# Kernel optimization log

Hardware: AMD Instinct MI355X
Metric: run time of the kernel (lower is better)

Reference implementation:

```python
import jax, jax.numpy as jnp
import numpy as np
from jax import lax

EPS = 1e-6
CLAMP = 1e4


def _ln_last(x, w, b):
    # fp32 LayerNorm over last dim
    mu = jnp.mean(x, axis=-1, keepdims=True)
    var = jnp.mean(jnp.square(x - mu), axis=-1, keepdims=True)
    return (x - mu) * lax.rsqrt(var + EPS) * w + b


def _nan_clean(x):
    return jnp.nan_to_num(x, nan=0.0, posinf=CLAMP, neginf=-CLAMP)


def setup_inputs() -> dict:
    key = jax.random.key(0)
    B, C, H, W = 4, 256, 64, 64
    hid = 2 * C  # expand=2
    k = 3        # d_conv
    ks = jax.random.split(key, 12)
    s = 0.02
    return {
        "x": jax.random.normal(ks[0], (B, C, H, W), jnp.float32),
        "ln2d_w": jnp.ones((C,), jnp.float32),
        "ln2d_b": jnp.zeros((C,), jnp.float32),
        "inproj_w": jax.random.normal(ks[1], (C, C), jnp.float32) * s,
        "inproj_b": jnp.zeros((C,), jnp.float32),
        "dw2d_w": jax.random.normal(ks[2], (C, 3, 3), jnp.float32) * s,
        "dw2d_b": jnp.zeros((C,), jnp.float32),
        "ssm_ln_w": jnp.ones((C,), jnp.float32),
        "ssm_ln_b": jnp.zeros((C,), jnp.float32),
        "ssm_in_w": jax.random.normal(ks[3], (2 * hid, C), jnp.float32) * s,
        "ssm_in_b": jnp.zeros((2 * hid,), jnp.float32),
        "ssm_dw_w": jax.random.normal(ks[4], (hid, k), jnp.float32) * s,
        "ssm_dw_b": jnp.zeros((hid,), jnp.float32),
        "ssm_out_w": jax.random.normal(ks[5], (C, hid), jnp.float32) * s,
        "ssm_out_b": jnp.zeros((C,), jnp.float32),
        "outproj_w": jax.random.normal(ks[6], (C, C), jnp.float32) * s,
        "outproj_b": jnp.zeros((C,), jnp.float32),
    }


def reference(x, ln2d_w, ln2d_b, inproj_w, inproj_b, dw2d_w, dw2d_b,
              ssm_ln_w, ssm_ln_b, ssm_in_w, ssm_in_b, ssm_dw_w, ssm_dw_b,
              ssm_out_w, ssm_out_b, outproj_w, outproj_b):
    B, C, H, W = x.shape
    L = H * W

    # LN2d over channel dim (per-pixel LN on C)
    y = _ln_last(x.transpose(0, 2, 3, 1), ln2d_w, ln2d_b).transpose(0, 3, 1, 2)

    # 1x1 conv in_proj
    y = jnp.einsum('bchw,oc->bohw', y, inproj_w) + inproj_b[None, :, None, None]

    # depthwise 3x3 conv, SAME padding
    y = lax.conv_general_dilated(
        y, dw2d_w[:, None, :, :], (1, 1), ((1, 1), (1, 1)),
        dimension_numbers=('NCHW', 'OIHW', 'NCHW'),
        feature_group_count=C) + dw2d_b[None, :, None, None]

    # cross-scan: 4 routes (B,L,C)
    s0 = y.reshape(B, C, L).transpose(0, 2, 1)                      # row-major
    s1 = s0[:, ::-1]                                                # reversed
    s2 = y.transpose(0, 1, 3, 2).reshape(B, C, L).transpose(0, 2, 1)  # col-major
    s3 = s2[:, ::-1]
    s = jnp.concatenate([s0, s1, s2, s3], axis=0)  # (4B, L, C), shared SSM weights

    # MambaOrLite fallback: LN -> GLU -> depthwise conv1d -> out proj + residual
    r = _ln_last(s, ssm_ln_w, ssm_ln_b)
    r = r @ ssm_in_w.T + ssm_in_b                   # (4B, L, 2*hid)
    a, g = jnp.split(r, 2, axis=-1)
    r = a * jax.nn.sigmoid(g)                       # (4B, L, hid)
    r = r.transpose(0, 2, 1)                        # (4B, hid, L)
    hid = r.shape[1]
    k = ssm_dw_w.shape[-1]
    pad = ((k - 1) // 2, k // 2)
    r = lax.conv_general_dilated(
        r, ssm_dw_w[:, None, :], (1,), (pad,),
        dimension_numbers=('NCH', 'OIH', 'NCH'),
        feature_group_count=hid) + ssm_dw_b[None, :, None]
    r = r.transpose(0, 2, 1) @ ssm_out_w.T + ssm_out_b  # (4B, L, C)
    ys = _nan_clean(r) + s

    # cross-merge: average the 4 routes back to (B,C,H,W)
    y0, y1, y2, y3 = jnp.split(ys, 4, axis=0)
    m0 = y0.transpose(0, 2, 1).reshape(B, C, H, W)
    m1 = y1[:, ::-1].transpose(0, 2, 1).reshape(B, C, H, W)
    m2 = y2.transpose(0, 2, 1).reshape(B, C, W, H).transpose(0, 1, 3, 2)
    m3 = y3[:, ::-1].transpose(0, 2, 1).reshape(B, C, W, H).transpose(0, 1, 3, 2)
    m = (m0 + m1 + m2 + m3) * 0.25

    out = jnp.einsum('bchw,oc->bohw', m, outproj_w) + outproj_b[None, :, None, None]
    out = _nan_clean(out)
    return out + x
```

## Files before the change

### kernel.cpp

```cpp
#include <hip/hip_runtime.h>

typedef float f32x4 __attribute__((ext_vector_type(4)));
typedef __bf16 bf16x8 __attribute__((ext_vector_type(8)));
typedef unsigned short u16;
typedef unsigned int u32;

__device__ __forceinline__ float bf2f(u32 b) {
  u32 x = (b & 0xffffu) << 16;
  return __builtin_bit_cast(float, x);
}
__device__ __forceinline__ u16 f2bf(float f) {
  u32 x = __builtin_bit_cast(u32, f);
  x += 0x7fffu + ((x >> 16) & 1u);
  return (u16)(x >> 16);
}
__device__ __forceinline__ void gload16(const void* g, void* l) {
  __builtin_amdgcn_global_load_lds((__attribute__((address_space(1))) void*)g,
                                   (__attribute__((address_space(3))) void*)l,
                                   16, 0, 0);
}
__device__ __forceinline__ int xcd_swz(int bid, int nwg) {
  int per = nwg >> 3;
  return (bid & 7) * per + (bid >> 3);
}

__global__ __launch_bounds__(256, 2)
void k_ln2d_prep(const float* __restrict__ x, const float* __restrict__ lw,
                 const float* __restrict__ lb, u16* __restrict__ A,
                 const float* __restrict__ inproj_w, const float* __restrict__ ssm_in_w,
                 const float* __restrict__ ssm_out_w, const float* __restrict__ outproj_w,
                 const float* __restrict__ dw2d_w, const float* __restrict__ ssm_dw_w,
                 const float* __restrict__ ssm_dw_b, const float* __restrict__ ssm_out_b,
                 u16* __restrict__ w1b, u16* __restrict__ w2b, u16* __restrict__ w3b,
                 u16* __restrict__ w4b, float* __restrict__ cvec, float* __restrict__ wT9,
                 float* __restrict__ w02, float* __restrict__ w14) {
  __shared__ float T[256 * 65];
  __shared__ float ps1[4][64], ps2[4][64];
  __shared__ float mu[64], rsd[64];
  int bid = blockIdx.x, tid = threadIdx.x;
  if (bid >= 256) {
    int pb = bid - 256;
    if (pb < 512) {
      const float* s; u16* d; int base;
      if (pb < 256)      { s = ssm_in_w;  d = w2b; base = pb; }
      else if (pb < 384) { s = ssm_out_w; d = w3b; base = pb - 256; }
      else if (pb < 448) { s = inproj_w;  d = w1b; base = pb - 384; }
      else               { s = outproj_w; d = w4b; base = pb - 448; }
      int i = base * 1024 + tid * 4;
      float4 v = *(const float4*)&s[i];
      u32 a = (u32)f2bf(v.x) | ((u32)f2bf(v.y) << 16);
      u32 b = (u32)f2bf(v.z) | ((u32)f2bf(v.w) << 16);
      *(uint2*)&d[i] = make_uint2(a, b);
    } else if (pb == 512) {
      float s = ssm_out_b[tid];
      const float* wr = ssm_out_w + (size_t)tid * 512;
      #pragma unroll 8
      for (int k = 0; k < 512; ++k) s += ssm_dw_b[k] * wr[k];
      cvec[tid] = s;
    } else {
      #pragma unroll
      for (int j = 0; j < 9; ++j) wT9[j * 256 + tid] = dw2d_w[tid * 9 + j];
      #pragma unroll
      for (int q = 0; q < 2; ++q) {
        int c = tid + q * 256;
        w02[c] = ssm_dw_w[c * 3 + 0] + ssm_dw_w[c * 3 + 2];
        w14[c] = 4.f * ssm_dw_w[c * 3 + 1];
      }
    }
    return;
  }
  int wv = tid >> 6, lane = tid & 63;
  int cq = lane >> 4, p4 = (lane & 15) * 4;
  int n0 = bid * 64, bb = n0 >> 12, hw0 = n0 & 4095;
  const float* xb = x + ((size_t)bb << 20);
  float s0 = 0, s1 = 0, s2 = 0, s3 = 0;
  float q0 = 0, q1 = 0, q2 = 0, q3 = 0;
  #pragma unroll 4
  for (int i = 0; i < 16; ++i) {
    int c = wv * 64 + i * 4 + cq;
    float4 v = *(const float4*)&xb[((size_t)c << 12) + hw0 + p4];
    T[c * 65 + p4 + 0] = v.x; T[c * 65 + p4 + 1] = v.y;
    T[c * 65 + p4 + 2] = v.z; T[c * 65 + p4 + 3] = v.w;
    s0 += v.x; s1 += v.y; s2 += v.z; s3 += v.w;
    q0 += v.x * v.x; q1 += v.y * v.y; q2 += v.z * v.z; q3 += v.w * v.w;
  }
  #pragma unroll
  for (int off = 16; off < 64; off <<= 1) {
    s0 += __shfl_xor(s0, off); s1 += __shfl_xor(s1, off);
    s2 += __shfl_xor(s2, off); s3 += __shfl_xor(s3, off);
    q0 += __shfl_xor(q0, off); q1 += __shfl_xor(q1, off);
    q2 += __shfl_xor(q2, off); q3 += __shfl_xor(q3, off);
  }
  if (cq == 0) {
    ps1[wv][p4 + 0] = s0; ps1[wv][p4 + 1] = s1; ps1[wv][p4 + 2] = s2; ps1[wv][p4 + 3] = s3;
    ps2[wv][p4 + 0] = q0; ps2[wv][p4 + 1] = q1; ps2[wv][p4 + 2] = q2; ps2[wv][p4 + 3] = q3;
  }
  __syncthreads();
  if (tid < 64) {
    float S1 = ps1[0][tid] + ps1[1][tid] + ps1[2][tid] + ps1[3][tid];
    float S2 = ps2[0][tid] + ps2[1][tid] + ps2[2][tid] + ps2[3][tid];
    float m = S1 * (1.f / 256.f);
    float var = S2 * (1.f / 256.f) - m * m;
    mu[tid] = m;
    rsd[tid] = rsqrtf(var + 1e-6f);
  }
  __syncthreads();
  int c4b = (tid & 15) * 4, p2b = tid >> 4;
  #pragma unroll
  for (int cc = 0; cc < 4; ++cc) {
    int c4 = cc * 64 + c4b;
    float4 w4 = *(const float4*)&lw[c4];
    float4 g4 = *(const float4*)&lb[c4];
    #pragma unroll
    for (int i2 = 0; i2 < 4; ++i2) {
      int p2 = p2b + 16 * i2;
      float m = mu[p2], rs = rsd[p2];
      float o0 = (T[(c4 + 0) * 65 + p2] - m) * rs * w4.x + g4.x;
      float o1 = (T[(c4 + 1) * 65 + p2] - m) * rs * w4.y + g4.y;
      float o2 = (T[(c4 + 2) * 65 + p2] - m) * rs * w4.z + g4.z;
      float o3 = (T[(c4 + 3) * 65 + p2] - m) * rs * w4.w + g4.w;
      u32 a = (u32)f2bf(o0) | ((u32)f2bf(o1) << 16);
      u32 b = (u32)f2bf(o2) | ((u32)f2bf(o3) << 16);
      *(uint2*)&A[(size_t)(n0 + p2) * 256 + c4] = make_uint2(a, b);
    }
  }
}

__global__ __launch_bounds__(256, 4)
void k_gemm_in(const u16* __restrict__ R, const u16* __restrict__ Cm,
               const float* __restrict__ bias, u16* __restrict__ outb) {
  __shared__ u16 tR[2][64 * 32];
  __shared__ u16 tC[2][128 * 32];
  int tid = threadIdx.x, lane = tid & 63, wv = tid >> 6;
  const int K = 256;
  int rt = blockIdx.x >> 1, ct = blockIdx.x & 1;
  int r0 = rt * 64, c0 = ct * 128;
  int fr = lane & 15, kc = lane >> 4;
  int sr = lane >> 2, sc = (lane & 3) * 8;
  f32x4 acc[4][2] = {};
  const u16* gR  = R  + (size_t)(r0 + wv * 16 + sr) * K + sc;
  const u16* gC0 = Cm + (size_t)(c0 + wv * 32 + sr) * K + sc;
  const u16* gC1 = Cm + (size_t)(c0 + wv * 32 + 16 + sr) * K + sc;
  auto STAGE = [&](int buf, int kt) {
    int k0 = kt * 32;
    gload16(gR + k0,  &tR[buf][wv * 16 * 32]);
    gload16(gC0 + k0, &tC[buf][(wv * 32) * 32]);
    gload16(gC1 + k0, &tC[buf][(wv * 32 + 16) * 32]);
  };
  auto COMPUTE = [&](int buf) {
    bf16x8 af[4], wf[2];
    #pragma unroll
    for (int m = 0; m < 4; ++m)
      af[m] = *(const bf16x8*)&tR[buf][(m * 16 + fr) * 32 + kc * 8];
    #pragma unroll
    for (int n = 0; n < 2; ++n)
      wf[n] = *(const bf16x8*)&tC[buf][(wv * 32 + n * 16 + fr) * 32 + kc * 8];
    #pragma unroll
    for (int m = 0; m < 4; ++m)
      #pragma unroll
      for (int n = 0; n < 2; ++n)
        acc[m][n] = __builtin_amdgcn_mfma_f32_16x16x32_bf16(af[m], wf[n], acc[m][n], 0, 0, 0);
  };
  STAGE(0, 0);
  __syncthreads();
  int cur = 0;
  for (int kt = 0; kt < 7; ++kt) {
    STAGE(cur ^ 1, kt + 1);
    __builtin_amdgcn_sched_barrier(0);
    COMPUTE(cur);
    __syncthreads();
    cur ^= 1;
  }
  COMPUTE(cur);
  #pragma unroll
  for (int m = 0; m < 4; ++m) {
    #pragma unroll
    for (int n = 0; n < 2; ++n) {
      #pragma unroll
      for (int r = 0; r < 4; ++r) {
        int gn = r0 + m * 16 + kc * 4 + r;
        int go = c0 + wv * 32 + n * 16 + fr;
        outb[(size_t)gn * 256 + go] = f2bf(acc[m][n][r] + bias[go]);
      }
    }
  }
}

__global__ __launch_bounds__(256)
void k_dw3x3_ln(const u16* __restrict__ Y1, const float* __restrict__ wT,
                const float* __restrict__ dwb, const float* __restrict__ lnw,
                const float* __restrict__ lnb, u16* __restrict__ Yc,
                u16* __restrict__ A) {
  int tid = threadIdx.x;
  int wg = xcd_swz(blockIdx.x, 4096);
  int n = wg * 4 + (tid >> 6);
  int lane = tid & 63;
  int c0 = lane * 4;
  int b = n >> 12, hw = n & 4095, h = hw >> 6, w = hw & 63;
  float4 b4 = *(const float4*)&dwb[c0];
  float a0 = b4.x, a1 = b4.y, a2 = b4.z, a3 = b4.w;
  #pragma unroll
  for (int ky = 0; ky < 3; ++ky) {
    int hh = h + ky - 1;
    if (hh < 0 || hh > 63) continue;
    #pragma unroll
    for (int kx = 0; kx < 3; ++kx) {
      int ww = w + kx - 1;
      if (ww < 0 || ww > 63) continue;
      size_t nn = ((size_t)b << 12) + (hh << 6) + ww;
      uint2 u = *(const uint2*)&Y1[nn * 256 + c0];
      float4 w4 = *(const float4*)&wT[(ky * 3 + kx) * 256 + c0];
      a0 += bf2f(u.x) * w4.x;
      a1 += bf2f(u.x >> 16) * w4.y;
      a2 += bf2f(u.y) * w4.z;
      a3 += bf2f(u.y >> 16) * w4.w;
    }
  }
  u32 p0 = (u32)f2bf(a0) | ((u32)f2bf(a1) << 16);
  u32 p1 = (u32)f2bf(a2) | ((u32)f2bf(a3) << 16);
  *(uint2*)&Yc[(size_t)n * 256 + c0] = make_uint2(p0, p1);
  float s1 = a0 + a1 + a2 + a3;
  float s2 = a0 * a0 + a1 * a1 + a2 * a2 + a3 * a3;
  #pragma unroll
  for (int off = 1; off < 64; off <<= 1) {
    s1 += __shfl_xor(s1, off);
    s2 += __shfl_xor(s2, off);
  }
  float m = s1 * (1.f / 256.f);
  float var = s2 * (1.f / 256.f) - m * m;
  float rs = rsqrtf(var + 1e-6f);
  float4 w4 = *(const float4*)&lnw[c0];
  float4 g4 = *(const float4*)&lnb[c0];
  float o0 = (a0 - m) * rs * w4.x + g4.x;
  float o1 = (a1 - m) * rs * w4.y + g4.y;
  float o2 = (a2 - m) * rs * w4.z + g4.z;
  float o3 = (a3 - m) * rs * w4.w + g4.w;
  u32 qa = (u32)f2bf(o0) | ((u32)f2bf(o1) << 16);
  u32 qb = (u32)f2bf(o2) | ((u32)f2bf(o3) << 16);
  *(uint2*)&A[(size_t)n * 256 + c0] = make_uint2(qa, qb);
}

__global__ __launch_bounds__(256, 3)
void k_gate2(const u16* __restrict__ A, const u16* __restrict__ W,
             const float* __restrict__ bias, u16* __restrict__ G) {
  __shared__ u16 tR[2][64 * 32];
  __shared__ u16 tCa[2][128 * 32];
  __shared__ u16 tCg[2][128 * 32];
  int tid = threadIdx.x, lane = tid & 63, wv = tid >> 6;
  int rt = blockIdx.x >> 2, ot = blockIdx.x & 3;
  int r0 = rt * 64, o0 = ot * 128;
  int fr = lane & 15, kc = lane >> 4;
  int sr = lane >> 2, sc = (lane & 3) * 8;
  const int K = 256;
  f32x4 acca[4][2] = {}, accg[4][2] = {};
  const u16* gR  = A + (size_t)(r0 + wv * 16 + sr) * K + sc;
  const u16* gA0 = W + (size_t)(o0 + wv * 32 + sr) * K + sc;
  const u16* gA1 = W + (size_t)(o0 + wv * 32 + 16 + sr) * K + sc;
  const u16* gG0 = W + (size_t)(512 + o0 + wv * 32 + sr) * K + sc;
  const u16* gG1 = W + (size_t)(512 + o0 + wv * 32 + 16 + sr) * K + sc;
  auto STAGE = [&](int buf, int kt) {
    int k0 = kt * 32;
    gload16(gR + k0,  &tR[buf][wv * 16 * 32]);
    gload16(gA0 + k0, &tCa[buf][(wv * 32) * 32]);
    gload16(gA1 + k0, &tCa[buf][(wv * 32 + 16) * 32]);
    gload16(gG0 + k0, &tCg[buf][(wv * 32) * 32]);
    gload16(gG1 + k0, &tCg[buf][(wv * 32 + 16) * 32]);
  };
  auto COMPUTE = [&](int buf) {
    bf16x8 af[4], wa[2], wg[2];
    #pragma unroll
    for (int m = 0; m < 4; ++m)
      af[m] = *(const bf16x8*)&tR[buf][(m * 16 + fr) * 32 + kc * 8];
    #pragma unroll
    for (int n = 0; n < 2; ++n) {
      wa[n] = *(const bf16x8*)&tCa[buf][(wv * 32 + n * 16 + fr) * 32 + kc * 8];
      wg[n] = *(const bf16x8*)&tCg[buf][(wv * 32 + n * 16 + fr) * 32 + kc * 8];
    }
    #pragma unroll
    for (int m = 0; m < 4; ++m)
      #pragma unroll
      for (int n = 0; n < 2; ++n) {
        acca[m][n] = __builtin_amdgcn_mfma_f32_16x16x32_bf16(af[m], wa[n], acca[m][n], 0, 0, 0);
        accg[m][n] = __builtin_amdgcn_mfma_f32_16x16x32_bf16(af[m], wg[n], accg[m][n], 0, 0, 0);
      }
  };
  STAGE(0, 0);
  __syncthreads();
  int cur = 0;
  for (int kt = 0; kt < 7; ++kt) {
    STAGE(cur ^ 1, kt + 1);
    __builtin_amdgcn_sched_barrier(0);
    COMPUTE(cur);
    __syncthreads();
    cur ^= 1;
  }
  COMPUTE(cur);
  #pragma unroll
  for (int m = 0; m < 4; ++m) {
    #pragma unroll
    for (int n = 0; n < 2; ++n) {
      #pragma unroll
      for (int r = 0; r < 4; ++r) {
        int gn = r0 + m * 16 + kc * 4 + r;
        int go = o0 + wv * 32 + n * 16 + fr;
        float a = acca[m][n][r] + bias[go];
        float g = accg[m][n][r] + bias[512 + go];
        G[(size_t)gn * 512 + go] = f2bf(a / (1.f + expf(-g)));
      }
    }
  }
}

__global__ __launch_bounds__(256, 2)
void k_scan_out(const u16* __restrict__ G, const u16* __restrict__ W3,
                const float* __restrict__ w02, const float* __restrict__ w14,
                const float* __restrict__ cvec, const u16* __restrict__ Yc,
                const u16* __restrict__ W4, const float* __restrict__ outb,
                const float* __restrict__ xres, float* __restrict__ out) {
  __shared__ u16 tR[2][32 * 32];
  __shared__ u16 tC[2][256 * 32];
  __shared__ u16 sM[32 * 256];
  int tid = threadIdx.x, lane = tid & 63, wv = tid >> 6;
  int wg = xcd_swz(blockIdx.x, 512);
  int r0 = wg * 32;
  int fr = lane & 15, kc = lane >> 4;
  int zrow = tid >> 3;
  int zg = (tid & 7) * 4;
  int n = r0 + zrow;
  int b = n >> 12, hw = n & 4095, h = hw >> 6, w = hw & 63;
  int m = w * 64 + h;
  int mm1 = m - 1, mp1 = m + 1;
  size_t o_c = (size_t)n * 512 + zg;
  size_t o_p = (size_t)(hw > 0 ? n - 1 : n) * 512 + zg;
  size_t o_n = (size_t)(hw < 4095 ? n + 1 : n) * 512 + zg;
  size_t o_u = (size_t)(m > 0 ? ((b << 12) + ((mm1 & 63) << 6) + (mm1 >> 6)) : n) * 512 + zg;
  size_t o_d = (size_t)(m < 4095 ? ((b << 12) + ((mp1 & 63) << 6) + (mp1 >> 6)) : n) * 512 + zg;
  float mP = hw > 0 ? 1.f : 0.f, mN = hw < 4095 ? 1.f : 0.f;
  float mU = m > 0 ? 1.f : 0.f, mD = m < 4095 ? 1.f : 0.f;
  f32x4 acc[2][4] = {};
  auto STAGE_C = [&](int buf, int kt) {
    int k0 = kt * 32;
    #pragma unroll
    for (int i = 0; i < 4; ++i) {
      int s0 = wv * 256 + i * 64;
      int s = s0 + lane;
      int row = s >> 2, off = (s & 3) * 8;
      gload16(W3 + (size_t)row * 512 + k0 + off, &tC[buf][s0 * 8]);
    }
  };
  uint2 lc, lp, ln_, lu, ld;
  float4 va, vb;
  auto ZLOAD = [&](int kt) {
    int c = kt * 32 + zg;
    lc  = *(const uint2*)&G[o_c + (kt * 32)];
    lp  = *(const uint2*)&G[o_p + (kt * 32)];
    ln_ = *(const uint2*)&G[o_n + (kt * 32)];
    lu  = *(const uint2*)&G[o_u + (kt * 32)];
    ld  = *(const uint2*)&G[o_d + (kt * 32)];
    va = *(const float4*)&w02[c];
    vb = *(const float4*)&w14[c];
  };
  auto ZSTORE = [&](int buf) {
    float s_0 = mP * bf2f(lp.x) + mN * bf2f(ln_.x) + mU * bf2f(lu.x) + mD * bf2f(ld.x);
    float s_1 = mP * bf2f(lp.x >> 16) + mN * bf2f(ln_.x >> 16) + mU * bf2f(lu.x >> 16) + mD * bf2f(ld.x >> 16);
    float s_2 = mP * bf2f(lp.y) + mN * bf2f(ln_.y) + mU * bf2f(lu.y) + mD * bf2f(ld.y);
    float s_3 = mP * bf2f(lp.y >> 16) + mN * bf2f(ln_.y >> 16) + mU * bf2f(lu.y >> 16) + mD * bf2f(ld.y >> 16);
    float z0 = va.x * s_0 + vb.x * bf2f(lc.x);
    float z1 = va.y * s_1 + vb.y * bf2f(lc.x >> 16);
    float z2 = va.z * s_2 + vb.z * bf2f(lc.y);
    float z3 = va.w * s_3 + vb.w * bf2f(lc.y >> 16);
    u32 p0 = (u32)f2bf(z0) | ((u32)f2bf(z1) << 16);
    u32 p1 = (u32)f2bf(z2) | ((u32)f2bf(z3) << 16);
    *(uint2*)&tR[buf][zrow * 32 + zg] = make_uint2(p0, p1);
  };
  auto COMPUTE = [&](int buf) {
    bf16x8 af[2], wf[4];
    #pragma unroll
    for (int mi = 0; mi < 2; ++mi)
      af[mi] = *(const bf16x8*)&tR[buf][(mi * 16 + fr) * 32 + kc * 8];
    #pragma unroll
    for (int ni = 0; ni < 4; ++ni)
      wf[ni] = *(const bf16x8*)&tC[buf][(wv * 64 + ni * 16 + fr) * 32 + kc * 8];
    #pragma unroll
    for (int mi = 0; mi < 2; ++mi)
      #pragma unroll
      for (int ni = 0; ni < 4; ++ni)
        acc[mi][ni] = __builtin_amdgcn_mfma_f32_16x16x32_bf16(af[mi], wf[ni], acc[mi][ni], 0, 0, 0);
  };
  STAGE_C(0, 0);
  ZLOAD(0);
  ZSTORE(0);
  __syncthreads();
  int cur = 0;
  for (int kt = 0; kt < 15; ++kt) {
    ZLOAD(kt + 1);
    STAGE_C(cur ^ 1, kt + 1);
    COMPUTE(cur);
    ZSTORE(cur ^ 1);
    __syncthreads();
    cur ^= 1;
  }
  COMPUTE(cur);
  #pragma unroll
  for (int mi = 0; mi < 2; ++mi) {
    #pragma unroll
    for (int ni = 0; ni < 4; ++ni) {
      #pragma unroll
      for (int r = 0; r < 4; ++r) {
        int row = mi * 16 + kc * 4 + r;
        int go = wv * 64 + ni * 16 + fr;
        float mval = 0.25f * acc[mi][ni][r] + cvec[go] +
                     bf2f(Yc[(size_t)(r0 + row) * 256 + go]);
        u32 ba = ((u32)(row * 512 + go * 2)) ^ ((u32)(row & 7) << 4);
        *(u16*)((char*)sM + ba) = f2bf(mval);
      }
    }
  }
  __syncthreads();
  f32x4 acc2[4][2] = {};
  #pragma unroll 2
  for (int kt = 0; kt < 8; ++kt) {
    bf16x8 af2[4], bfv[2];
    #pragma unroll
    for (int mi = 0; mi < 4; ++mi)
      af2[mi] = *(const bf16x8*)&W4[(size_t)(wv * 64 + mi * 16 + fr) * 256 + kt * 32 + kc * 8];
    #pragma unroll
    for (int ni = 0; ni < 2; ++ni) {
      int pos = ni * 16 + fr;
      u32 ba = ((u32)(pos * 512 + (kt * 32 + kc * 8) * 2)) ^ ((u32)(pos & 7) << 4);
      bfv[ni] = *(const bf16x8*)((const char*)sM + ba);
    }
    #pragma unroll
    for (int mi = 0; mi < 4; ++mi)
      #pragma unroll
      for (int ni = 0; ni < 2; ++ni)
        acc2[mi][ni] = __builtin_amdgcn_mfma_f32_16x16x32_bf16(af2[mi], bfv[ni], acc2[mi][ni], 0, 0, 0);
  }
  int bb = r0 >> 12, hwb = r0 & 4095;
  #pragma unroll
  for (int mi = 0; mi < 4; ++mi) {
    #pragma unroll
    for (int ni = 0; ni < 2; ++ni) {
      #pragma unroll
      for (int r = 0; r < 4; ++r) {
        int o = wv * 64 + mi * 16 + kc * 4 + r;
        int pos = ni * 16 + fr;
        size_t idx = (((size_t)(bb * 256 + o)) << 12) + hwb + pos;
        float res = __builtin_nontemporal_load(&xres[idx]);
        __builtin_nontemporal_store(acc2[mi][ni][r] + outb[o] + res, &out[idx]);
      }
    }
  }
}

extern "C" void kernel_launch(void* const* d_in, const int* in_sizes, int n_in,
                              void* d_out, int out_size, void* d_ws, size_t ws_size,
                              hipStream_t stream) {
  const float* x         = (const float*)d_in[0];
  const float* ln2d_w    = (const float*)d_in[1];
  const float* ln2d_b    = (const float*)d_in[2];
  const float* inproj_w  = (const float*)d_in[3];
  const float* inproj_b  = (const float*)d_in[4];
  const float* dw2d_w    = (const float*)d_in[5];
  const float* dw2d_b    = (const float*)d_in[6];
  const float* ssm_ln_w  = (const float*)d_in[7];
  const float* ssm_ln_b  = (const float*)d_in[8];
  const float* ssm_in_w  = (const float*)d_in[9];
  const float* ssm_in_b  = (const float*)d_in[10];
  const float* ssm_dw_w  = (const float*)d_in[11];
  const float* ssm_dw_b  = (const float*)d_in[12];
  const float* ssm_out_w = (const float*)d_in[13];
  const float* ssm_out_b = (const float*)d_in[14];
  const float* outproj_w = (const float*)d_in[15];
  const float* outproj_b = (const float*)d_in[16];
  float* out = (float*)d_out;

  char* ws = (char*)d_ws;
  size_t off = 0;
  auto take = [&](size_t bytes) -> char* {
    char* p = ws + off;
    off = (off + bytes + 255) & ~(size_t)255;
    return p;
  };
  u16* w1b    = (u16*)take(65536 * 2);
  u16* w2b    = (u16*)take(262144 * 2);
  u16* w3b    = (u16*)take(131072 * 2);
  u16* w4b    = (u16*)take(65536 * 2);
  float* cvec = (float*)take(256 * 4);
  float* wT9  = (float*)take(9 * 256 * 4);
  float* w02  = (float*)take(512 * 4);
  float* w14  = (float*)take(512 * 4);
  u16* Abuf   = (u16*)take((size_t)16384 * 256 * 2);
  u16* Y1     = (u16*)take((size_t)16384 * 256 * 2);
  u16* Yc     = (u16*)take((size_t)16384 * 256 * 2);
  u16* G      = (u16*)take((size_t)16384 * 512 * 2);
  (void)ws_size; (void)in_sizes; (void)n_in; (void)out_size;

  k_ln2d_prep<<<770, 256, 0, stream>>>(x, ln2d_w, ln2d_b, Abuf,
                                       inproj_w, ssm_in_w, ssm_out_w, outproj_w,
                                       dw2d_w, ssm_dw_w, ssm_dw_b, ssm_out_b,
                                       w1b, w2b, w3b, w4b, cvec, wT9, w02, w14);
  k_gemm_in<<<512, 256, 0, stream>>>(Abuf, w1b, inproj_b, Y1);
  k_dw3x3_ln<<<4096, 256, 0, stream>>>(Y1, wT9, dw2d_b, ssm_ln_w, ssm_ln_b, Yc, Abuf);
  k_gate2<<<1024, 256, 0, stream>>>(Abuf, w2b, ssm_in_b, G);
  k_scan_out<<<512, 256, 0, stream>>>(G, w3b, w02, w14, cvec, Yc,
                                      w4b, outproj_b, x, out);
}
```

Baseline: 109.6 us.

## Replace in-proj and gate GEMMs with row-tile kernel looping over all output columns

Both the in_proj GEMM and the gated ssm_in GEMM are replaced by one templated kernel. Each block now loads a 32-row slab of activations into LDS once and loops over all output column tiles, streaming weight tiles through a double buffer, so activation rows are read from global memory only once. LDS uses XOR-swizzled layouts to avoid bank conflicts, and outputs are staged in LDS for coalesced 16-byte stores. The price is smaller per-block MFMA tiles (2x2), more LDS per block and lower occupancy, plus repeated weight re-reads per block.

```diff
diff --git a/kernel.cpp b/kernel.cpp
--- a/kernel.cpp
+++ b/kernel.cpp
@@ -126,63 +126,102 @@
   }
 }
 
-__global__ __launch_bounds__(256, 4)
-void k_gemm_in(const u16* __restrict__ R, const u16* __restrict__ Cm,
-               const float* __restrict__ bias, u16* __restrict__ outb) {
-  __shared__ u16 tR[2][64 * 32];
-  __shared__ u16 tC[2][128 * 32];
+template <int NOT, bool GATE>
+__global__ __launch_bounds__(256, 2)
+void k_colgemm(const u16* __restrict__ A, const u16* __restrict__ W,
+               const float* __restrict__ bias, u16* __restrict__ Out) {
+  constexpr int COLS = NOT * 128;
+  __shared__ u16 sA[32 * 256];
+  __shared__ u16 tCa[2][128 * 32];
+  __shared__ u16 tCg[(GATE ? 2 : 1)][128 * 32];
+  __shared__ u16 sO[32 * COLS];
   int tid = threadIdx.x, lane = tid & 63, wv = tid >> 6;
-  const int K = 256;
-  int rt = blockIdx.x >> 1, ct = blockIdx.x & 1;
-  int r0 = rt * 64, c0 = ct * 128;
+  int r0 = blockIdx.x * 32;
   int fr = lane & 15, kc = lane >> 4;
-  int sr = lane >> 2, sc = (lane & 3) * 8;
-  f32x4 acc[4][2] = {};
-  const u16* gR  = R  + (size_t)(r0 + wv * 16 + sr) * K + sc;
-  const u16* gC0 = Cm + (size_t)(c0 + wv * 32 + sr) * K + sc;
-  const u16* gC1 = Cm + (size_t)(c0 + wv * 32 + 16 + sr) * K + sc;
-  auto STAGE = [&](int buf, int kt) {
-    int k0 = kt * 32;
-    gload16(gR + k0,  &tR[buf][wv * 16 * 32]);
-    gload16(gC0 + k0, &tC[buf][(wv * 32) * 32]);
-    gload16(gC1 + k0, &tC[buf][(wv * 32 + 16) * 32]);
-  };
-  auto COMPUTE = [&](int buf) {
-    bf16x8 af[4], wf[2];
-    #pragma unroll
-    for (int m = 0; m < 4; ++m)
-      af[m] = *(const bf16x8*)&tR[buf][(m * 16 + fr) * 32 + kc * 8];
-    #pragma unroll
-    for (int n = 0; n < 2; ++n)
-      wf[n] = *(const bf16x8*)&tC[buf][(wv * 32 + n * 16 + fr) * 32 + kc * 8];
-    #pragma unroll
-    for (int m = 0; m < 4; ++m)
-      #pragma unroll
-      for (int n = 0; n < 2; ++n)
-        acc[m][n] = __builtin_amdgcn_mfma_f32_16x16x32_bf16(af[m], wf[n], acc[m][n], 0, 0, 0);
-  };
-  STAGE(0, 0);
-  __syncthreads();
-  int cur = 0;
-  for (int kt = 0; kt < 7; ++kt) {
-    STAGE(cur ^ 1, kt + 1);
-    __builtin_amdgcn_sched_barrier(0);
-    COMPUTE(cur);
-    __syncthreads();
-    cur ^= 1;
-  }
-  COMPUTE(cur);
-  #pragma unroll
-  for (int m = 0; m < 4; ++m) {
-    #pragma unroll
-    for (int n = 0; n < 2; ++n) {
-      #pragma unroll
-      for (int r = 0; r < 4; ++r) {
-        int gn = r0 + m * 16 + kc * 4 + r;
-        int go = c0 + wv * 32 + n * 16 + fr;
-        outb[(size_t)gn * 256 + go] = f2bf(acc[m][n][r] + bias[go]);
-      }
-    }
+  #pragma unroll
+  for (int j = 0; j < 4; ++j) {
+    int Gi0 = j * 256 + wv * 64;
+    int Gi = Gi0 + lane;
+    int row = Gi >> 5, g = Gi & 31;
+    gload16(A + (size_t)(r0 + row) * 256 + ((g ^ (row & 7)) << 3), &sA[Gi0 * 8]);
+  }
+  auto STAGE_W = [&](int buf, int ot, int kt) {
+    #pragma unroll
+    for (int j = 0; j < 2; ++j) {
+      int Gi0 = j * 256 + wv * 64;
+      int Gi = Gi0 + lane;
+      int row = Gi >> 2, g = Gi & 3;
+      int gs = (g ^ ((row >> 1) & 3)) << 3;
+      gload16(W + (size_t)(ot * 128 + row) * 256 + kt * 32 + gs, &tCa[buf][Gi0 * 8]);
+      if constexpr (GATE)
+        gload16(W + (size_t)(512 + ot * 128 + row) * 256 + kt * 32 + gs, &tCg[buf][Gi0 * 8]);
+    }
+  };
+  STAGE_W(0, 0, 0);
+  __syncthreads();
+  int buf = 0;
+  for (int ot = 0; ot < NOT; ++ot) {
+    f32x4 aA[2][2] = {};
+    f32x4 aG[2][2] = {};
+    for (int kt = 0; kt < 8; ++kt) {
+      int np = ot * 8 + kt + 1;
+      if (np < NOT * 8) STAGE_W(buf ^ 1, np >> 3, np & 7);
+      __builtin_amdgcn_sched_barrier(0);
+      bf16x8 af[2], wa[2], wg[2];
+      #pragma unroll
+      for (int m = 0; m < 2; ++m) {
+        int row = m * 16 + fr;
+        af[m] = *(const bf16x8*)&sA[row * 256 + (((kt * 4 + kc) ^ (fr & 7)) << 3)];
+      }
+      int wgs = (kc ^ ((fr >> 1) & 3)) << 3;
+      #pragma unroll
+      for (int n = 0; n < 2; ++n) {
+        int row = wv * 32 + n * 16 + fr;
+        wa[n] = *(const bf16x8*)&tCa[buf][row * 32 + wgs];
+        if constexpr (GATE)
+          wg[n] = *(const bf16x8*)&tCg[buf][row * 32 + wgs];
+      }
+      #pragma unroll
+      for (int m = 0; m < 2; ++m)
+        #pragma unroll
+        for (int n = 0; n < 2; ++n) {
+          aA[m][n] = __builtin_amdgcn_mfma_f32_16x16x32_bf16(af[m], wa[n], aA[m][n], 0, 0, 0);
+          if constexpr (GATE)
+            aG[m][n] = __builtin_amdgcn_mfma_f32_16x16x32_bf16(af[m], wg[n], aG[m][n], 0, 0, 0);
+        }
+      __syncthreads();
+      buf ^= 1;
+    }
+    #pragma unroll
+    for (int m = 0; m < 2; ++m) {
+      #pragma unroll
+      for (int n = 0; n < 2; ++n) {
+        #pragma unroll
+        for (int r = 0; r < 4; ++r) {
+          int row = m * 16 + kc * 4 + r;
+          int go = ot * 128 + wv * 32 + n * 16 + fr;
+          float v;
+          if constexpr (GATE) {
+            float a = aA[m][n][r] + bias[go];
+            float g = aG[m][n][r] + bias[512 + go];
+            v = a / (1.f + expf(-g));
+          } else {
+            v = aA[m][n][r] + bias[go];
+          }
+          sO[row * COLS + go] = f2bf(v);
+        }
+      }
+    }
+  }
+  __syncthreads();
+  constexpr int GPR = COLS / 8;
+  constexpr int NG = 32 * GPR;
+  #pragma unroll
+  for (int j = 0; j < NG / 256; ++j) {
+    int Gi = j * 256 + wv * 64 + lane;
+    int row = Gi / GPR, cg = Gi % GPR;
+    uint4 v = *(const uint4*)&sO[Gi * 8];
+    *(uint4*)&Out[(size_t)(r0 + row) * COLS + cg * 8] = v;
   }
 }
 
@@ -238,77 +277,6 @@
   u32 qa = (u32)f2bf(o0) | ((u32)f2bf(o1) << 16);
   u32 qb = (u32)f2bf(o2) | ((u32)f2bf(o3) << 16);
   *(uint2*)&A[(size_t)n * 256 + c0] = make_uint2(qa, qb);
-}
-
-__global__ __launch_bounds__(256, 3)
-void k_gate2(const u16* __restrict__ A, const u16* __restrict__ W,
-             const float* __restrict__ bias, u16* __restrict__ G) {
-  __shared__ u16 tR[2][64 * 32];
-  __shared__ u16 tCa[2][128 * 32];
-  __shared__ u16 tCg[2][128 * 32];
-  int tid = threadIdx.x, lane = tid & 63, wv = tid >> 6;
-  int rt = blockIdx.x >> 2, ot = blockIdx.x & 3;
-  int r0 = rt * 64, o0 = ot * 128;
-  int fr = lane & 15, kc = lane >> 4;
-  int sr = lane >> 2, sc = (lane & 3) * 8;
-  const int K = 256;
-  f32x4 acca[4][2] = {}, accg[4][2] = {};
-  const u16* gR  = A + (size_t)(r0 + wv * 16 + sr) * K + sc;
-  const u16* gA0 = W + (size_t)(o0 + wv * 32 + sr) * K + sc;
-  const u16* gA1 = W + (size_t)(o0 + wv * 32 + 16 + sr) * K + sc;
-  const u16* gG0 = W + (size_t)(512 + o0 + wv * 32 + sr) * K + sc;
-  const u16* gG1 = W + (size_t)(512 + o0 + wv * 32 + 16 + sr) * K + sc;
-  auto STAGE = [&](int buf, int kt) {
-    int k0 = kt * 32;
-    gload16(gR + k0,  &tR[buf][wv * 16 * 32]);
-    gload16(gA0 + k0, &tCa[buf][(wv * 32) * 32]);
-    gload16(gA1 + k0, &tCa[buf][(wv * 32 + 16) * 32]);
-    gload16(gG0 + k0, &tCg[buf][(wv * 32) * 32]);
-    gload16(gG1 + k0, &tCg[buf][(wv * 32 + 16) * 32]);
-  };
-  auto COMPUTE = [&](int buf) {
-    bf16x8 af[4], wa[2], wg[2];
-    #pragma unroll
-    for (int m = 0; m < 4; ++m)
-      af[m] = *(const bf16x8*)&tR[buf][(m * 16 + fr) * 32 + kc * 8];
-    #pragma unroll
-    for (int n = 0; n < 2; ++n) {
-      wa[n] = *(const bf16x8*)&tCa[buf][(wv * 32 + n * 16 + fr) * 32 + kc * 8];
-      wg[n] = *(const bf16x8*)&tCg[buf][(wv * 32 + n * 16 + fr) * 32 + kc * 8];
-    }
-    #pragma unroll
-    for (int m = 0; m < 4; ++m)
-      #pragma unroll
-      for (int n = 0; n < 2; ++n) {
-        acca[m][n] = __builtin_amdgcn_mfma_f32_16x16x32_bf16(af[m], wa[n], acca[m][n], 0, 0, 0);
-        accg[m][n] = __builtin_amdgcn_mfma_f32_16x16x32_bf16(af[m], wg[n], accg[m][n], 0, 0, 0);
-      }
-  };
-  STAGE(0, 0);
-  __syncthreads();
-  int cur = 0;
-  for (int kt = 0; kt < 7; ++kt) {
-    STAGE(cur ^ 1, kt + 1);
-    __builtin_amdgcn_sched_barrier(0);
-    COMPUTE(cur);
-    __syncthreads();
-    cur ^= 1;
-  }
-  COMPUTE(cur);
-  #pragma unroll
-  for (int m = 0; m < 4; ++m) {
-    #pragma unroll
-    for (int n = 0; n < 2; ++n) {
-      #pragma unroll
-      for (int r = 0; r < 4; ++r) {
-        int gn = r0 + m * 16 + kc * 4 + r;
-        int go = o0 + wv * 32 + n * 16 + fr;
-        float a = acca[m][n][r] + bias[go];
-        float g = accg[m][n][r] + bias[512 + go];
-        G[(size_t)gn * 512 + go] = f2bf(a / (1.f + expf(-g)));
-      }
-    }
-  }
 }
 
 __global__ __launch_bounds__(256, 2)
@@ -500,9 +468,9 @@
                                        inproj_w, ssm_in_w, ssm_out_w, outproj_w,
                                        dw2d_w, ssm_dw_w, ssm_dw_b, ssm_out_b,
                                        w1b, w2b, w3b, w4b, cvec, wT9, w02, w14);
-  k_gemm_in<<<512, 256, 0, stream>>>(Abuf, w1b, inproj_b, Y1);
+  k_colgemm<2, false><<<512, 256, 0, stream>>>(Abuf, w1b, inproj_b, Y1);
   k_dw3x3_ln<<<4096, 256, 0, stream>>>(Y1, wT9, dw2d_b, ssm_ln_w, ssm_ln_b, Yc, Abuf);
-  k_gate2<<<1024, 256, 0, stream>>>(Abuf, w2b, ssm_in_b, G);
+  k_colgemm<4, true><<<512, 256, 0, stream>>>(Abuf, w2b, ssm_in_b, G);
   k_scan_out<<<512, 256, 0, stream>>>(G, w3b, w02, w14, cvec, Yc,
                                       w4b, outproj_b, x, out);
 }
```

Measured after the change: 115.6 us. +5.4%, slower.
